# Kernel tuning notes

Measured on AMD Instinct MI355X. Metric: run time of the kernel, lower is better.

## Reference

```python
import jax, jax.numpy as jnp
import numpy as np

VOCAB = 128
HIDDEN = 1024

def setup_inputs() -> dict:
    key = jax.random.key(0)
    kx, ku, kw, kl, kb = jax.random.split(key, 5)
    B, S = 64, 512
    X = jax.random.randint(kx, (B, S), 0, VOCAB)
    # xavier_uniform bounds
    bu = float(np.sqrt(6.0 / (HIDDEN + HIDDEN)))
    bw = float(np.sqrt(6.0 / (HIDDEN + VOCAB)))
    U = jax.random.uniform(ku, (HIDDEN, HIDDEN), minval=-bu, maxval=bu, dtype=jnp.float32)
    W = jax.random.uniform(kw, (HIDDEN, VOCAB), minval=-bw, maxval=bw, dtype=jnp.float32)
    # nn.Linear(hidden, vocab): weight [vocab, hidden], bias [vocab]
    bl = float(1.0 / np.sqrt(HIDDEN))
    lin_w = jax.random.uniform(kl, (VOCAB, HIDDEN), minval=-bl, maxval=bl, dtype=jnp.float32)
    lin_b = jax.random.uniform(kb, (VOCAB,), minval=-bl, maxval=bl, dtype=jnp.float32)
    return {"X": X, "U": U, "W": W, "lin_w": lin_w, "lin_b": lin_b}

def reference(X, U, W, lin_w, lin_b):
    B, S = X.shape
    # one-hot embedding (use_embedding=False path)
    X_emb = jax.nn.one_hot(X, VOCAB, dtype=jnp.float32)  # [B,S,V]
    # precompute input contribution for all steps: x_t @ W.T -> [B,S,H]
    inp = jnp.einsum('bsv,hv->bsh', X_emb, W)
    h0 = jnp.zeros((B, HIDDEN), dtype=jnp.float32)

    def step(h, inp_t):
        h_new = jnp.tanh(h @ U.T + inp_t)  # [B,H]
        return h_new, h_new

    _, hs = jax.lax.scan(step, h0, jnp.swapaxes(inp, 0, 1))  # hs: [S,B,H]
    hs = jnp.swapaxes(hs, 0, 1)  # [B,S,H]
    logits = jnp.einsum('bsh,vh->bsv', hs, lin_w) + lin_b  # [B,S,V]
    return jax.nn.softmax(logits, axis=-1)
```

## Files before the change

kernel.cpp:

```cpp
#include <hip/hip_runtime.h>
#include <cstdint>

typedef float f32x4 __attribute__((ext_vector_type(4)));

static constexpr int Hdim = 1024;
static constexpr int Vdim = 128;
static constexpr int Bdim = 64;
static constexpr int Sdim = 512;

static constexpr int NB   = 8;
static constexpr int NI   = 32;
static constexpr int KCH  = 32;
static constexpr int SL   = 1028;
static constexpr int NBLK = 256;
static constexpr int BPC  = 32;
static constexpr int NCL  = 8;

__global__ void __launch_bounds__(256) pack_u_kernel(const float* __restrict__ U,
                                                     float* __restrict__ Up) {
  __shared__ float tile[32][257];
  const int s  = blockIdx.x;
  const int k0 = blockIdx.y * 256;
  const int t  = threadIdx.x;
  #pragma unroll
  for (int r = 0; r < 32; ++r)
    tile[r][t] = U[(size_t)(s * 32 + r) * Hdim + k0 + t];
  __syncthreads();
  const size_t base = ((size_t)s * Hdim + k0) * 32;
  #pragma unroll
  for (int r2 = 0; r2 < 32; ++r2) {
    int g = r2 * 256 + t;
    Up[base + g] = tile[g & 31][g >> 5];
  }
}

__global__ void transpose_w_kernel(const float* __restrict__ in, float* __restrict__ out) {
  __shared__ float tile[32][33];
  const int bx = blockIdx.x * 32;
  const int by = blockIdx.y * 32;
  const int tx = threadIdx.x, ty = threadIdx.y;
  #pragma unroll
  for (int dy = 0; dy < 32; dy += 8)
    tile[ty + dy][tx] = in[(size_t)(by + ty + dy) * Vdim + bx + tx];
  __syncthreads();
  #pragma unroll
  for (int dy = 0; dy < 32; dy += 8)
    out[(size_t)(bx + ty + dy) * Hdim + by + tx] = tile[tx][ty + dy];
}

__global__ void __launch_bounds__(256, 1) rnn_persist_kernel(
    const float* __restrict__ Up,
    const float* __restrict__ Wt,
    const int*   __restrict__ X,
    const float* __restrict__ lw,
    const float* __restrict__ lb,
    float* __restrict__ h0,
    float* __restrict__ h1,
    unsigned int* __restrict__ flags,
    float* __restrict__ out)
{
  __shared__ float hsm[NB * SL];
  __shared__ float part[4][NB][NI];
  __shared__ float partv[4][NB][4];

  const int tid  = threadIdx.x;
  const int blk  = blockIdx.x;
  const int cl   = blk >> 5;
  const int s    = blk & 31;
  const int i0   = s * NI;
  const int bg0  = cl * NB;
  const int kp   = tid >> 3;
  const int b    = tid & 7;
  const int w    = tid >> 6;
  const int lane = tid & 63;
  const float* Ublk = Up + (size_t)s * Hdim * NI;

  auto stage_h = [&](int t) {
    if (t == 0) {
      const f32x4 z = (f32x4){0.f, 0.f, 0.f, 0.f};
      #pragma unroll
      for (int r = 0; r < NB; ++r)
        *((f32x4*)&hsm[r * SL + tid * 4]) = z;
    } else {
      const float* hc = (t & 1) ? h1 : h0;
      const float* p = hc + (size_t)bg0 * Hdim + tid * 4;
      f32x4 v0, v1, v2, v3, v4, v5, v6, v7;
      asm volatile(
          "global_load_dwordx4 %0, %8, off sc0 sc1\n\t"
          "global_load_dwordx4 %1, %9, off sc0 sc1\n\t"
          "global_load_dwordx4 %2, %10, off sc0 sc1\n\t"
          "global_load_dwordx4 %3, %11, off sc0 sc1\n\t"
          "global_load_dwordx4 %4, %12, off sc0 sc1\n\t"
          "global_load_dwordx4 %5, %13, off sc0 sc1\n\t"
          "global_load_dwordx4 %6, %14, off sc0 sc1\n\t"
          "global_load_dwordx4 %7, %15, off sc0 sc1\n\t"
          "s_waitcnt vmcnt(0)"
          : "=&v"(v0), "=&v"(v1), "=&v"(v2), "=&v"(v3),
            "=&v"(v4), "=&v"(v5), "=&v"(v6), "=&v"(v7)
          : "v"(p), "v"(p + Hdim), "v"(p + 2 * Hdim), "v"(p + 3 * Hdim),
            "v"(p + 4 * Hdim), "v"(p + 5 * Hdim), "v"(p + 6 * Hdim), "v"(p + 7 * Hdim)
          : "memory");
      *((f32x4*)&hsm[0 * SL + tid * 4]) = v0;
      *((f32x4*)&hsm[1 * SL + tid * 4]) = v1;
      *((f32x4*)&hsm[2 * SL + tid * 4]) = v2;
      *((f32x4*)&hsm[3 * SL + tid * 4]) = v3;
      *((f32x4*)&hsm[4 * SL + tid * 4]) = v4;
      *((f32x4*)&hsm[5 * SL + tid * 4]) = v5;
      *((f32x4*)&hsm[6 * SL + tid * 4]) = v6;
      *((f32x4*)&hsm[7 * SL + tid * 4]) = v7;
    }
  };

  auto logits_partial = [&]() {
    float a0 = 0.f, a1 = 0.f, a2 = 0.f, a3 = 0.f;
    const f32x4* lw0 = (const f32x4*)(lw + (size_t)(4 * s)     * Hdim + kp * KCH);
    const f32x4* lw1 = (const f32x4*)(lw + (size_t)(4 * s + 1) * Hdim + kp * KCH);
    const f32x4* lw2 = (const f32x4*)(lw + (size_t)(4 * s + 2) * Hdim + kp * KCH);
    const f32x4* lw3 = (const f32x4*)(lw + (size_t)(4 * s + 3) * Hdim + kp * KCH);
    const f32x4* hr4 = (const f32x4*)&hsm[b * SL + kp * KCH];
    #pragma unroll
    for (int j = 0; j < KCH / 4; ++j) {
      int jj = (j + kp) & (KCH / 4 - 1);
      f32x4 hv = hr4[jj];
      f32x4 q0 = lw0[jj], q1 = lw1[jj], q2 = lw2[jj], q3 = lw3[jj];
      #pragma unroll
      for (int e = 0; e < 4; ++e) {
        a0 += hv[e] * q0[e]; a1 += hv[e] * q1[e];
        a2 += hv[e] * q2[e]; a3 += hv[e] * q3[e];
      }
    }
    #pragma unroll
    for (int d = 8; d < 64; d <<= 1) {
      a0 += __shfl_xor(a0, d, 64); a1 += __shfl_xor(a1, d, 64);
      a2 += __shfl_xor(a2, d, 64); a3 += __shfl_xor(a3, d, 64);
    }
    if ((lane & 56) == 0)
      *((f32x4*)&partv[w][b][0]) = (f32x4){a0, a1, a2, a3};
  };

  auto logits_combine = [&](int tt) {
    if (tid >= 128 && tid < 128 + 4 * NB) {
      const int q = tid - 128;
      const int bb = q >> 2, vv = q & 3;
      float lv = partv[0][bb][vv] + partv[1][bb][vv] + partv[2][bb][vv] + partv[3][bb][vv];
      lv += lb[4 * s + vv];
      out[((size_t)(bg0 + bb) * Sdim + tt) * Vdim + 4 * s + vv] = lv;
    }
  };

  for (int t = 0; t < Sdim; ++t) {
    stage_h(t);
    __syncthreads();

    {
      float acc[NI];
      #pragma unroll
      for (int i = 0; i < NI; ++i) acc[i] = 0.f;
      const float* hr = &hsm[b * SL + kp * KCH];
      const f32x4* ub = (const f32x4*)(Ublk + (size_t)kp * KCH * NI);
      #pragma unroll 4
      for (int j = 0; j < KCH; ++j) {
        int jj = (j + kp) & (KCH - 1);
        float hv = hr[jj];
        const f32x4* u = ub + (size_t)jj * (NI / 4);
        #pragma unroll
        for (int q = 0; q < NI / 4; ++q) {
          const f32x4 uq = u[q];
          acc[q * 4 + 0] += uq[0] * hv;
          acc[q * 4 + 1] += uq[1] * hv;
          acc[q * 4 + 2] += uq[2] * hv;
          acc[q * 4 + 3] += uq[3] * hv;
        }
      }
      #pragma unroll
      for (int i = 0; i < NI; ++i) {
        acc[i] += __shfl_xor(acc[i], 8, 64);
        acc[i] += __shfl_xor(acc[i], 16, 64);
        acc[i] += __shfl_xor(acc[i], 32, 64);
      }
      if ((lane & 56) == 0) {
        #pragma unroll
        for (int i = 0; i < NI; i += 4)
          *((f32x4*)&part[w][b][i]) = (f32x4){acc[i], acc[i + 1], acc[i + 2], acc[i + 3]};
      }
    }
    __syncthreads();

    {
      const int b2 = tid >> 5, i2 = tid & 31;
      float v = part[0][b2][i2] + part[1][b2][i2] + part[2][b2][i2] + part[3][b2][i2];
      const int x = X[(bg0 + b2) * Sdim + t];
      v += Wt[(size_t)x * Hdim + i0 + i2];
      v = tanhf(v);
      float* hn = (t & 1) ? h0 : h1;
      __hip_atomic_store(&hn[(size_t)(bg0 + b2) * Hdim + i0 + i2], v,
                         __ATOMIC_RELAXED, __HIP_MEMORY_SCOPE_SYSTEM);
    }

    asm volatile("s_waitcnt vmcnt(0)" ::: "memory");
    __syncthreads();
    if (tid == 0)
      __hip_atomic_store(&flags[cl * BPC + s], (unsigned)(t + 1),
                         __ATOMIC_RELAXED, __HIP_MEMORY_SCOPE_SYSTEM);

    if (t > 0) logits_partial();
    __syncthreads();
    if (t > 0) logits_combine(t - 1);

    if (tid < 64) {
      const unsigned int tag = (unsigned)(t + 1);
      unsigned int* f = &flags[cl * BPC + (tid & (BPC - 1))];
      while (true) {
        unsigned int fv = __hip_atomic_load(f, __ATOMIC_RELAXED, __HIP_MEMORY_SCOPE_SYSTEM);
        if (__all((int)(fv >= tag))) break;
        __builtin_amdgcn_s_sleep(1);
      }
    }
    __syncthreads();
  }

  stage_h(Sdim);
  __syncthreads();
  logits_partial();
  __syncthreads();
  logits_combine(Sdim - 1);
}

__global__ void __launch_bounds__(256) softmax_kernel(float* __restrict__ out) {
  const int row = blockIdx.x * 4 + (threadIdx.x >> 6);
  const int l = threadIdx.x & 63;
  float* rp = out + (size_t)row * Vdim;
  float2 v = *((const float2*)&rp[l * 2]);
  float m = fmaxf(v.x, v.y);
  #pragma unroll
  for (int d = 1; d < 64; d <<= 1) m = fmaxf(m, __shfl_xor(m, d, 64));
  float e0 = expf(v.x - m), e1 = expf(v.y - m);
  float ss = e0 + e1;
  #pragma unroll
  for (int d = 1; d < 64; d <<= 1) ss += __shfl_xor(ss, d, 64);
  const float inv = 1.f / ss;
  *((float2*)&rp[l * 2]) = make_float2(e0 * inv, e1 * inv);
}

extern "C" void kernel_launch(void* const* d_in, const int* in_sizes, int n_in,
                              void* d_out, int out_size, void* d_ws, size_t ws_size,
                              hipStream_t stream) {
  const int*   X  = (const int*)d_in[0];
  const float* U  = (const float*)d_in[1];
  const float* W  = (const float*)d_in[2];
  const float* lw = (const float*)d_in[3];
  const float* lb = (const float*)d_in[4];
  float* out = (float*)d_out;

  float* Up = (float*)d_ws;
  float* Wt = Up + (size_t)1024 * 1024;
  float* h0 = Wt + (size_t)128 * 1024;
  float* h1 = h0 + (size_t)64 * 1024;
  unsigned int* flags = (unsigned int*)(h1 + (size_t)64 * 1024);
  const size_t need = ((size_t)1024 * 1024 + 128 * 1024 + 2 * 64 * 1024) * 4 + NCL * BPC * 4;
  if (ws_size < need) return;

  hipMemsetAsync(flags, 0, (size_t)NCL * BPC * sizeof(unsigned int), stream);

  hipLaunchKernelGGL(pack_u_kernel, dim3(32, 4), dim3(256), 0, stream, U, Up);
  hipLaunchKernelGGL(transpose_w_kernel, dim3(4, 32), dim3(32, 8), 0, stream, W, Wt);

  void* args[] = {(void*)&Up, (void*)&Wt, (void*)&X, (void*)&lw, (void*)&lb,
                  (void*)&h0, (void*)&h1, (void*)&flags, (void*)&out};
  hipError_t ce = hipLaunchCooperativeKernel((void*)rnn_persist_kernel,
                                             dim3(NBLK), dim3(256), args, 0, stream);
  if (ce != hipSuccess) {
    hipLaunchKernelGGL(rnn_persist_kernel, dim3(NBLK), dim3(256), 0, stream,
                       Up, Wt, X, lw, lb, h0, h1, flags, out);
  }

  hipLaunchKernelGGL(softmax_kernel, dim3((Bdim * Sdim) / 4), dim3(256), 0, stream, out);
}
```

Before: 6.360 ms.

## Halve persistent RNN block count by giving each block 64 hidden outputs

Each persistent block now computes 64 hidden units instead of 32, so each batch cluster needs 16 blocks rather than 32 and the grid drops from 256 to 128 blocks. The U packing, the logits slice (8 vocab rows per block) and the reduction/store logic are adjusted to match. The aim is to cut per-step cross-block flag synchronization and the redundant staging of h, since fewer blocks each load the full hidden state. In exchange each block does twice the FMA work per step with doubled register accumulators, and only half the CUs are used.

```diff
diff --git a/kernel.cpp b/kernel.cpp
--- a/kernel.cpp
+++ b/kernel.cpp
@@ -9,28 +9,29 @@
 static constexpr int Sdim = 512;
 
 static constexpr int NB   = 8;
-static constexpr int NI   = 32;
+static constexpr int NI   = 64;
 static constexpr int KCH  = 32;
 static constexpr int SL   = 1028;
-static constexpr int NBLK = 256;
-static constexpr int BPC  = 32;
+static constexpr int NBLK = 128;
+static constexpr int BPC  = 16;
 static constexpr int NCL  = 8;
 
 __global__ void __launch_bounds__(256) pack_u_kernel(const float* __restrict__ U,
                                                      float* __restrict__ Up) {
   __shared__ float tile[32][257];
-  const int s  = blockIdx.x;
-  const int k0 = blockIdx.y * 256;
-  const int t  = threadIdx.x;
+  const int sh   = blockIdx.x;
+  const int s    = sh >> 1, half = sh & 1;
+  const int k0   = blockIdx.y * 256;
+  const int t    = threadIdx.x;
   #pragma unroll
   for (int r = 0; r < 32; ++r)
-    tile[r][t] = U[(size_t)(s * 32 + r) * Hdim + k0 + t];
-  __syncthreads();
-  const size_t base = ((size_t)s * Hdim + k0) * 32;
+    tile[r][t] = U[(size_t)(s * 64 + half * 32 + r) * Hdim + k0 + t];
+  __syncthreads();
   #pragma unroll
   for (int r2 = 0; r2 < 32; ++r2) {
-    int g = r2 * 256 + t;
-    Up[base + g] = tile[g & 31][g >> 5];
+    int g  = r2 * 256 + t;
+    int il = g & 31, kr = g >> 5;
+    Up[((size_t)s * Hdim + k0 + kr) * 64 + half * 32 + il] = tile[il][kr];
   }
 }
 
@@ -61,12 +62,12 @@
 {
   __shared__ float hsm[NB * SL];
   __shared__ float part[4][NB][NI];
-  __shared__ float partv[4][NB][4];
+  __shared__ float partv[4][NB][8];
 
   const int tid  = threadIdx.x;
   const int blk  = blockIdx.x;
-  const int cl   = blk >> 5;
-  const int s    = blk & 31;
+  const int cl   = blk >> 4;
+  const int s    = blk & 15;
   const int i0   = s * NI;
   const int bg0  = cl * NB;
   const int kp   = tid >> 3;
@@ -112,39 +113,43 @@
   };
 
   auto logits_partial = [&]() {
-    float a0 = 0.f, a1 = 0.f, a2 = 0.f, a3 = 0.f;
-    const f32x4* lw0 = (const f32x4*)(lw + (size_t)(4 * s)     * Hdim + kp * KCH);
-    const f32x4* lw1 = (const f32x4*)(lw + (size_t)(4 * s + 1) * Hdim + kp * KCH);
-    const f32x4* lw2 = (const f32x4*)(lw + (size_t)(4 * s + 2) * Hdim + kp * KCH);
-    const f32x4* lw3 = (const f32x4*)(lw + (size_t)(4 * s + 3) * Hdim + kp * KCH);
+    float a[8];
+    #pragma unroll
+    for (int r = 0; r < 8; ++r) a[r] = 0.f;
     const f32x4* hr4 = (const f32x4*)&hsm[b * SL + kp * KCH];
     #pragma unroll
-    for (int j = 0; j < KCH / 4; ++j) {
-      int jj = (j + kp) & (KCH / 4 - 1);
-      f32x4 hv = hr4[jj];
-      f32x4 q0 = lw0[jj], q1 = lw1[jj], q2 = lw2[jj], q3 = lw3[jj];
-      #pragma unroll
-      for (int e = 0; e < 4; ++e) {
-        a0 += hv[e] * q0[e]; a1 += hv[e] * q1[e];
-        a2 += hv[e] * q2[e]; a3 += hv[e] * q3[e];
-      }
+    for (int r = 0; r < 8; ++r) {
+      const f32x4* lwr = (const f32x4*)(lw + (size_t)(8 * s + r) * Hdim + kp * KCH);
+      float ar = 0.f;
+      #pragma unroll
+      for (int j = 0; j < KCH / 4; ++j) {
+        int jj = (j + kp) & (KCH / 4 - 1);
+        f32x4 hv = hr4[jj];
+        f32x4 qv = lwr[jj];
+        #pragma unroll
+        for (int e = 0; e < 4; ++e) ar += hv[e] * qv[e];
+      }
+      a[r] = ar;
     }
     #pragma unroll
-    for (int d = 8; d < 64; d <<= 1) {
-      a0 += __shfl_xor(a0, d, 64); a1 += __shfl_xor(a1, d, 64);
-      a2 += __shfl_xor(a2, d, 64); a3 += __shfl_xor(a3, d, 64);
-    }
-    if ((lane & 56) == 0)
-      *((f32x4*)&partv[w][b][0]) = (f32x4){a0, a1, a2, a3};
+    for (int r = 0; r < 8; ++r) {
+      a[r] += __shfl_xor(a[r], 8, 64);
+      a[r] += __shfl_xor(a[r], 16, 64);
+      a[r] += __shfl_xor(a[r], 32, 64);
+    }
+    if ((lane & 56) == 0) {
+      *((f32x4*)&partv[w][b][0]) = (f32x4){a[0], a[1], a[2], a[3]};
+      *((f32x4*)&partv[w][b][4]) = (f32x4){a[4], a[5], a[6], a[7]};
+    }
   };
 
   auto logits_combine = [&](int tt) {
-    if (tid >= 128 && tid < 128 + 4 * NB) {
+    if (tid >= 128 && tid < 192) {
       const int q = tid - 128;
-      const int bb = q >> 2, vv = q & 3;
+      const int bb = q >> 3, vv = q & 7;
       float lv = partv[0][bb][vv] + partv[1][bb][vv] + partv[2][bb][vv] + partv[3][bb][vv];
-      lv += lb[4 * s + vv];
-      out[((size_t)(bg0 + bb) * Sdim + tt) * Vdim + 4 * s + vv] = lv;
+      lv += lb[8 * s + vv];
+      out[((size_t)(bg0 + bb) * Sdim + tt) * Vdim + 8 * s + vv] = lv;
     }
   };
 
@@ -158,7 +163,7 @@
       for (int i = 0; i < NI; ++i) acc[i] = 0.f;
       const float* hr = &hsm[b * SL + kp * KCH];
       const f32x4* ub = (const f32x4*)(Ublk + (size_t)kp * KCH * NI);
-      #pragma unroll 4
+      #pragma unroll 2
       for (int j = 0; j < KCH; ++j) {
         int jj = (j + kp) & (KCH - 1);
         float hv = hr[jj];
@@ -188,12 +193,18 @@
 
     {
       const int b2 = tid >> 5, i2 = tid & 31;
-      float v = part[0][b2][i2] + part[1][b2][i2] + part[2][b2][i2] + part[3][b2][i2];
+      float v1 = part[0][b2][i2] + part[1][b2][i2] + part[2][b2][i2] + part[3][b2][i2];
+      float v2 = part[0][b2][i2 + 32] + part[1][b2][i2 + 32] +
+                 part[2][b2][i2 + 32] + part[3][b2][i2 + 32];
       const int x = X[(bg0 + b2) * Sdim + t];
-      v += Wt[(size_t)x * Hdim + i0 + i2];
-      v = tanhf(v);
+      v1 += Wt[(size_t)x * Hdim + i0 + i2];
+      v2 += Wt[(size_t)x * Hdim + i0 + 32 + i2];
+      v1 = tanhf(v1);
+      v2 = tanhf(v2);
       float* hn = (t & 1) ? h0 : h1;
-      __hip_atomic_store(&hn[(size_t)(bg0 + b2) * Hdim + i0 + i2], v,
+      __hip_atomic_store(&hn[(size_t)(bg0 + b2) * Hdim + i0 + i2], v1,
+                         __ATOMIC_RELAXED, __HIP_MEMORY_SCOPE_SYSTEM);
+      __hip_atomic_store(&hn[(size_t)(bg0 + b2) * Hdim + i0 + 32 + i2], v2,
                          __ATOMIC_RELAXED, __HIP_MEMORY_SCOPE_SYSTEM);
     }
 
```

Result: slower. 11.70 ms (+84.0%).
